# Optimization experiments

Measured on AMD Instinct MI355X. Metric: run time of the kernel, lower is better.

## Reference

```python
import jax, jax.numpy as jnp
import numpy as np
import math

TAU = 2.0
EPS = 1e-5
ALPHA = 2.0  # spikingjelly surrogate.ATan default alpha

@jax.custom_vjp
def atan_spike(x):
    return (x >= 0.0).astype(x.dtype)

def _spike_fwd(x):
    return atan_spike(x), x

def _spike_bwd(x, g):
    s = math.pi / 2.0 * ALPHA
    return (g * (ALPHA / 2.0) / (1.0 + (s * x) ** 2),)

atan_spike.defvjp(_spike_fwd, _spike_bwd)

def lif_seq(x_seq):
    # MultiStepLIFNode: v' = v + (x - v)/tau ; spike = H(v'-1) ; hard reset to v_reset=0
    def step(v, x):
        v = v + (x - v) / TAU
        s = atan_spike(v - 1.0)
        v = v * (1.0 - jax.lax.stop_gradient(s))  # detach_reset=True
        return v, s
    _, s_seq = jax.lax.scan(step, jnp.zeros_like(x_seq[0]), x_seq)
    return s_seq

def setup_inputs() -> dict:
    key = jax.random.key(0)
    kx, kw = jax.random.split(key)
    T, B, N, P, D = 4, 64, 1024, 63, 128
    x = jax.random.normal(kx, (T, B, N, P), dtype=jnp.float32)
    W = jax.random.normal(kw, (D, P), dtype=jnp.float32) * np.float32(1.0 / np.sqrt(P))
    gamma = jnp.ones((D,), dtype=jnp.float32)
    beta = jnp.zeros((D,), dtype=jnp.float32)
    return {"x": x, "W": W, "gamma": gamma, "beta": beta, "pe": 0}

def reference(x, W, gamma, beta, pe):
    # bias-free Linear: [T,B,N,P] x [D,P] -> [T,B,N,D]
    h = jnp.einsum('tbnp,dp->tbnd', x, W)
    # BatchNorm1d over channel D; training-mode batch stats over (T*B, N)
    mean = jnp.mean(h, axis=(0, 1, 2), keepdims=True)
    var = jnp.var(h, axis=(0, 1, 2), keepdims=True)  # biased, as torch BN normalization
    h = (h - mean) * jax.lax.rsqrt(var + EPS) * gamma + beta
    # multi-step LIF across T (self.pe=False -> tAPE branch skipped)
    out = lif_seq(h)  # [T,B,N,D] == original output after final transpose
    return out
```

## Files before the change

kernel.cpp:

```cpp
#include <hip/hip_runtime.h>
#include <math.h>

#define T_STEPS 4
#define R_ROWS  65536
#define M_ROWS  262144
#define P_DIM   63
#define D_DIM   128
#define PP      64

#define TILES_TOTAL (M_ROWS / 64)
#define G_CHUNKS 8

__global__ __launch_bounds__(256) void gram_kernel(const float* __restrict__ x,
                                                   double* __restrict__ partials,
                                                   int tiles_per_block) {
    __shared__ __align__(16) float xt[2][64 * PP];
    const int tid = threadIdx.x;
    const int tj = tid & 15;
    const int ti = tid >> 4;

    double dacc[4][4];
#pragma unroll
    for (int a = 0; a < 4; a++)
#pragma unroll
        for (int b = 0; b < 4; b++) dacc[a][b] = 0.0;

    if (tid < 64) {
        xt[0][tid * PP + 63] = 1.0f;
        xt[1][tid * PP + 63] = 1.0f;
    }

    const int tile0 = blockIdx.x * tiles_per_block;
    float4 reg[4];

    {
        const float4* src = (const float4*)(x + (size_t)tile0 * (64 * 63));
#pragma unroll
        for (int it = 0; it < 4; it++) {
            int k = tid + it * 256;
            reg[it] = (k < 1008) ? src[k] : make_float4(0.f, 0.f, 0.f, 0.f);
        }
    }
#pragma unroll
    for (int it = 0; it < 4; it++) {
        int k = tid + it * 256;
        if (k < 1008) {
            const float* ve = (const float*)&reg[it];
            int flat = k * 4;
#pragma unroll
            for (int e = 0; e < 4; e++) {
                int f = flat + e;
                int r = f / 63;
                int c = f - r * 63;
                xt[0][r * PP + c] = ve[e];
            }
        }
    }
    __syncthreads();

    for (int t = 0; t < tiles_per_block; t++) {
        const int cur = t & 1;
        if (t + 1 < tiles_per_block) {
            const float4* src = (const float4*)(x + (size_t)(tile0 + t + 1) * (64 * 63));
#pragma unroll
            for (int it = 0; it < 4; it++) {
                int k = tid + it * 256;
                reg[it] = (k < 1008) ? src[k] : make_float4(0.f, 0.f, 0.f, 0.f);
            }
        }

        float facc[4][4];
#pragma unroll
        for (int a = 0; a < 4; a++)
#pragma unroll
            for (int b = 0; b < 4; b++) facc[a][b] = 0.0f;

        const float* buf = xt[cur];
        for (int r = 0; r < 64; r++) {
            float4 xi = *(const float4*)&buf[r * PP + ti * 4];
            float4 xj = *(const float4*)&buf[r * PP + tj * 4];
            const float* xia = (const float*)&xi;
            const float* xja = (const float*)&xj;
#pragma unroll
            for (int a = 0; a < 4; a++)
#pragma unroll
                for (int b = 0; b < 4; b++)
                    facc[a][b] = fmaf(xia[a], xja[b], facc[a][b]);
        }
#pragma unroll
        for (int a = 0; a < 4; a++)
#pragma unroll
            for (int b = 0; b < 4; b++) dacc[a][b] += (double)facc[a][b];

        __syncthreads();
        if (t + 1 < tiles_per_block) {
            float* nbuf = xt[1 - cur];
#pragma unroll
            for (int it = 0; it < 4; it++) {
                int k = tid + it * 256;
                if (k < 1008) {
                    const float* ve = (const float*)&reg[it];
                    int flat = k * 4;
#pragma unroll
                    for (int e = 0; e < 4; e++) {
                        int f = flat + e;
                        int r = f / 63;
                        int c = f - r * 63;
                        nbuf[r * PP + c] = ve[e];
                    }
                }
            }
            __syncthreads();
        }
    }

    double* Pb = partials + (size_t)blockIdx.x * 4096;
#pragma unroll
    for (int a = 0; a < 4; a++)
#pragma unroll
        for (int b = 0; b < 4; b++)
            Pb[(ti * 4 + a) * 64 + (tj * 4 + b)] = dacc[a][b];
}

__global__ __launch_bounds__(256) void reduce_kernel(const double* __restrict__ partials,
                                                     double* __restrict__ G8,
                                                     int copies_per_chunk) {
    const int chunk = blockIdx.x >> 4;
    const int idx   = (blockIdx.x & 15) * 256 + threadIdx.x;
    const double* src = partials + (size_t)chunk * copies_per_chunk * 4096;
    double s = 0.0;
    for (int c = 0; c < copies_per_chunk; c++)
        s += src[(size_t)c * 4096 + idx];
    G8[(size_t)chunk * 4096 + idx] = s;
}

__global__ __launch_bounds__(64) void stats_kernel(const double* __restrict__ G,
                                                   const float* __restrict__ W,
                                                   const float* __restrict__ gamma,
                                                   const float* __restrict__ beta,
                                                   float* __restrict__ stats) {
    const int d = blockIdx.x;
    const int p = threadIdx.x;
    __shared__ float sW[64];
    sW[p] = (p < P_DIM) ? W[d * P_DIM + p] : 0.0f;
    __syncthreads();

    double inner = 0.0;
#pragma unroll
    for (int c = 0; c < G_CHUNKS; c++) {
        const double* Gr = G + (size_t)c * (64 * 64) + p * 64;
        for (int q = 0; q < 64; q++) inner += Gr[q] * (double)sW[q];
    }

    double contrib = (double)sW[p] * inner;
    double ex2M = contrib;
#pragma unroll
    for (int off = 32; off > 0; off >>= 1) ex2M += __shfl_down(ex2M, off, 64);
    double meanM = __shfl(inner, 63, 64);

    if (p == 0) {
        double mean = meanM / (double)M_ROWS;
        double ex2  = ex2M  / (double)M_ROWS;
        double var  = ex2 - mean * mean;
        float varf  = (float)var;
        float vpe   = varf + 1e-5f;
        float invstd = (float)(1.0 / sqrt((double)vpe));
        stats[d * 4 + 0] = (float)mean;
        stats[d * 4 + 1] = invstd;
        stats[d * 4 + 2] = gamma[d];
        stats[d * 4 + 3] = beta[d];
    }
}

#define LIF_ROWS 16
#define SW_STRIDE 132
__global__ __launch_bounds__(256) void lif_kernel(const float* __restrict__ x,
                                                  const float* __restrict__ W,
                                                  const float* __restrict__ stats,
                                                  float* __restrict__ out) {
    __shared__ __align__(16) float sw[P_DIM * SW_STRIDE];
    __shared__ __align__(16) float sx[T_STEPS * LIF_ROWS * P_DIM + 4];
    const int tid = threadIdx.x;

    for (int k = tid; k < P_DIM * D_DIM; k += 256) {
        int d = k / 63;
        int p = k - d * 63;
        sw[p * SW_STRIDE + d] = W[k];
    }

    const int r0 = blockIdx.x * LIF_ROWS;
    const int seg = tid >> 6;
    const int lane = tid & 63;
    const float4* src = (const float4*)(x + ((size_t)seg * R_ROWS + r0) * P_DIM);
    float4* dst = (float4*)sx + seg * 252;
    for (int k = lane; k < 252; k += 64) {
        dst[k] = src[k];
    }
    __syncthreads();

    const int td = tid & 31;
    const int tr = tid >> 5;
    const int d0 = td * 4;
    const int rowa = tr * 2;

    float acc[T_STEPS][2][4];
#pragma unroll
    for (int t = 0; t < T_STEPS; t++)
#pragma unroll
        for (int i = 0; i < 2; i++)
#pragma unroll
            for (int j = 0; j < 4; j++) acc[t][i][j] = 0.0f;

    for (int p = 0; p < P_DIM; p++) {
        float4 w4 = *(const float4*)&sw[p * SW_STRIDE + d0];
#pragma unroll
        for (int t = 0; t < T_STEPS; t++)
#pragma unroll
            for (int i = 0; i < 2; i++) {
                float xv = sx[(t * LIF_ROWS + rowa + i) * P_DIM + p];
                acc[t][i][0] = fmaf(xv, w4.x, acc[t][i][0]);
                acc[t][i][1] = fmaf(xv, w4.y, acc[t][i][1]);
                acc[t][i][2] = fmaf(xv, w4.z, acc[t][i][2]);
                acc[t][i][3] = fmaf(xv, w4.w, acc[t][i][3]);
            }
    }

#pragma unroll
    for (int i = 0; i < 2; i++) {
        const int row = r0 + rowa + i;
        float sval[T_STEPS][4];
#pragma unroll
        for (int j = 0; j < 4; j++) {
            float4 st = ((const float4*)stats)[d0 + j];
            float v = 0.0f;
#pragma unroll
            for (int t = 0; t < T_STEPS; t++) {
                float hn = (acc[t][i][j] - st.x) * st.y;
                hn = hn * st.z;
                hn = hn + st.w;
                v = v + (hn - v) * 0.5f;
                float s = (v >= 1.0f) ? 1.0f : 0.0f;
                sval[t][j] = s;
                if (s != 0.0f) v = 0.0f;
            }
        }
#pragma unroll
        for (int t = 0; t < T_STEPS; t++) {
            float4 o = make_float4(sval[t][0], sval[t][1], sval[t][2], sval[t][3]);
            *(float4*)&out[((size_t)t * R_ROWS + row) * D_DIM + d0] = o;
        }
    }
}

extern "C" void kernel_launch(void* const* d_in, const int* in_sizes, int n_in,
                              void* d_out, int out_size, void* d_ws, size_t ws_size,
                              hipStream_t stream) {
    const float* x     = (const float*)d_in[0];
    const float* W     = (const float*)d_in[1];
    const float* gamma = (const float*)d_in[2];
    const float* beta  = (const float*)d_in[3];
    float* out = (float*)d_out;

    const size_t fixed = (size_t)G_CHUNKS * 4096 * 8 + 4096;
    int nparts = 512;
    while (nparts > 64 && (size_t)nparts * 4096 * 8 + fixed > ws_size) nparts >>= 1;
    const int tiles_per_block = TILES_TOTAL / nparts;

    double* partials = (double*)d_ws;
    double* G8       = (double*)((char*)d_ws + (size_t)nparts * 4096 * 8);
    float*  stats    = (float*)((char*)G8 + (size_t)G_CHUNKS * 4096 * 8);

    gram_kernel<<<nparts, 256, 0, stream>>>(x, partials, tiles_per_block);
    reduce_kernel<<<G_CHUNKS * 16, 256, 0, stream>>>(partials, G8, nparts / G_CHUNKS);
    stats_kernel<<<D_DIM, 64, 0, stream>>>(G8, W, gamma, beta, stats);
    lif_kernel<<<R_ROWS / LIF_ROWS, 256, 0, stream>>>(x, W, stats, out);
}
```

Measured before the change: 290.7 us.

## Enlarge LIF tile to 32 rows with swizzled float4 LDS loads of x

The LIF GEMM kernel now handles 32 rows per block, and each thread computes 8 output columns instead of 4. x is stored in LDS padded to 64 columns with an XOR swizzle, so the inner loop can read float4 vectors of x and four p-values of W per step. This cuts LDS read instructions per FMA and halves the grid size. It also doubles the accumulator registers (64 floats) and the per-block LDS footprint, which may lower occupancy. W is transposed through LDS using an extra staging pass.

```diff
diff --git a/kernel.cpp b/kernel.cpp
--- a/kernel.cpp
+++ b/kernel.cpp
@@ -172,65 +172,116 @@
     }
 }
 
-#define LIF_ROWS 16
-#define SW_STRIDE 132
-__global__ __launch_bounds__(256) void lif_kernel(const float* __restrict__ x,
-                                                  const float* __restrict__ W,
-                                                  const float* __restrict__ stats,
-                                                  float* __restrict__ out) {
-    __shared__ __align__(16) float sw[P_DIM * SW_STRIDE];
-    __shared__ __align__(16) float sx[T_STEPS * LIF_ROWS * P_DIM + 4];
+#define LIF_ROWS 32
+__global__ __launch_bounds__(256, 2) void lif_kernel(const float* __restrict__ x,
+                                                     const float* __restrict__ W,
+                                                     const float* __restrict__ stats,
+                                                     float* __restrict__ out) {
+    __shared__ __align__(16) float sw[P_DIM * D_DIM];
+    __shared__ __align__(16) float sx[T_STEPS * LIF_ROWS * 64];
     const int tid = threadIdx.x;
 
+    for (int k = tid; k < P_DIM * D_DIM; k += 256) sx[k] = W[k];
+    __syncthreads();
     for (int k = tid; k < P_DIM * D_DIM; k += 256) {
-        int d = k / 63;
-        int p = k - d * 63;
-        sw[p * SW_STRIDE + d] = W[k];
-    }
+        int p = k >> 7;
+        int d = k & 127;
+        sw[k] = sx[d * P_DIM + p];
+    }
+    __syncthreads();
 
     const int r0 = blockIdx.x * LIF_ROWS;
     const int seg = tid >> 6;
     const int lane = tid & 63;
     const float4* src = (const float4*)(x + ((size_t)seg * R_ROWS + r0) * P_DIM);
-    float4* dst = (float4*)sx + seg * 252;
-    for (int k = lane; k < 252; k += 64) {
-        dst[k] = src[k];
-    }
-    __syncthreads();
-
-    const int td = tid & 31;
-    const int tr = tid >> 5;
-    const int d0 = td * 4;
-    const int rowa = tr * 2;
-
-    float acc[T_STEPS][2][4];
+    for (int k = lane; k < 504; k += 64) {
+        float4 v = src[k];
+        const float* ve = (const float*)&v;
+        int flat = k * 4;
+#pragma unroll
+        for (int e = 0; e < 4; e++) {
+            int f = flat + e;
+            int r = f / 63;
+            int c = f - r * 63;
+            int cs = (((c >> 2) ^ ((r >> 1) & 3)) << 2) | (c & 3);
+            sx[(seg * LIF_ROWS + r) * 64 + cs] = ve[e];
+        }
+    }
+    __syncthreads();
+
+    const int td = tid & 15;
+    const int tr = tid >> 4;
+    const int d0 = td * 8;
+    const int lr0 = tr * 2;
+    const int sq0 = (lr0 >> 1) & 3;
+
+    float acc[T_STEPS][2][8];
 #pragma unroll
     for (int t = 0; t < T_STEPS; t++)
 #pragma unroll
         for (int i = 0; i < 2; i++)
 #pragma unroll
-            for (int j = 0; j < 4; j++) acc[t][i][j] = 0.0f;
-
-    for (int p = 0; p < P_DIM; p++) {
-        float4 w4 = *(const float4*)&sw[p * SW_STRIDE + d0];
+            for (int j = 0; j < 8; j++) acc[t][i][j] = 0.0f;
+
+    for (int pq = 0; pq < 15; pq++) {
+        const int p0 = pq * 4;
+        float4 w[4][2];
+#pragma unroll
+        for (int pp = 0; pp < 4; pp++)
+#pragma unroll
+            for (int h = 0; h < 2; h++)
+                w[pp][h] = *(const float4*)&sw[(p0 + pp) * D_DIM + d0 + h * 4];
+
+        const int xq = (pq ^ sq0) << 2;
 #pragma unroll
         for (int t = 0; t < T_STEPS; t++)
 #pragma unroll
             for (int i = 0; i < 2; i++) {
-                float xv = sx[(t * LIF_ROWS + rowa + i) * P_DIM + p];
-                acc[t][i][0] = fmaf(xv, w4.x, acc[t][i][0]);
-                acc[t][i][1] = fmaf(xv, w4.y, acc[t][i][1]);
-                acc[t][i][2] = fmaf(xv, w4.z, acc[t][i][2]);
-                acc[t][i][3] = fmaf(xv, w4.w, acc[t][i][3]);
+                float4 xv = *(const float4*)&sx[(t * LIF_ROWS + lr0 + i) * 64 + xq];
+                const float xe[4] = {xv.x, xv.y, xv.z, xv.w};
+                float* a = acc[t][i];
+#pragma unroll
+                for (int pp = 0; pp < 4; pp++) {
+#pragma unroll
+                    for (int h = 0; h < 2; h++) {
+                        const float4 ww = w[pp][h];
+                        a[h * 4 + 0] = fmaf(xe[pp], ww.x, a[h * 4 + 0]);
+                        a[h * 4 + 1] = fmaf(xe[pp], ww.y, a[h * 4 + 1]);
+                        a[h * 4 + 2] = fmaf(xe[pp], ww.z, a[h * 4 + 2]);
+                        a[h * 4 + 3] = fmaf(xe[pp], ww.w, a[h * 4 + 3]);
+                    }
+                }
+            }
+    }
+
+#pragma unroll
+    for (int p = 60; p < 63; p++) {
+        float4 wA = *(const float4*)&sw[p * D_DIM + d0];
+        float4 wB = *(const float4*)&sw[p * D_DIM + d0 + 4];
+        const int cs = ((15 ^ sq0) << 2) | (p & 3);
+#pragma unroll
+        for (int t = 0; t < T_STEPS; t++)
+#pragma unroll
+            for (int i = 0; i < 2; i++) {
+                float xv = sx[(t * LIF_ROWS + lr0 + i) * 64 + cs];
+                float* a = acc[t][i];
+                a[0] = fmaf(xv, wA.x, a[0]);
+                a[1] = fmaf(xv, wA.y, a[1]);
+                a[2] = fmaf(xv, wA.z, a[2]);
+                a[3] = fmaf(xv, wA.w, a[3]);
+                a[4] = fmaf(xv, wB.x, a[4]);
+                a[5] = fmaf(xv, wB.y, a[5]);
+                a[6] = fmaf(xv, wB.z, a[6]);
+                a[7] = fmaf(xv, wB.w, a[7]);
             }
     }
 
 #pragma unroll
     for (int i = 0; i < 2; i++) {
-        const int row = r0 + rowa + i;
-        float sval[T_STEPS][4];
-#pragma unroll
-        for (int j = 0; j < 4; j++) {
+        const int row = r0 + lr0 + i;
+        float sval[T_STEPS][8];
+#pragma unroll
+        for (int j = 0; j < 8; j++) {
             float4 st = ((const float4*)stats)[d0 + j];
             float v = 0.0f;
 #pragma unroll
@@ -246,8 +297,9 @@
         }
 #pragma unroll
         for (int t = 0; t < T_STEPS; t++) {
-            float4 o = make_float4(sval[t][0], sval[t][1], sval[t][2], sval[t][3]);
-            *(float4*)&out[((size_t)t * R_ROWS + row) * D_DIM + d0] = o;
+            float* ob = &out[((size_t)t * R_ROWS + row) * D_DIM + d0];
+            *(float4*)ob       = make_float4(sval[t][0], sval[t][1], sval[t][2], sval[t][3]);
+            *(float4*)(ob + 4) = make_float4(sval[t][4], sval[t][5], sval[t][6], sval[t][7]);
         }
     }
 }
```

Measured after the change: 291.7 us. No clear change (+0.3%).

## Use packed FP32 FMA with row-interleaved shared layout and nontemporal memory ops

Applied to the files above, without the earlier changes.

Shared-memory x is re-laid out so the two rows a thread handles are interleaved per column. Each thread can then feed v_pk_fma_f32 through inline asm with op_sel broadcast of the weights, halving FMA instruction count and cutting LDS reads via wider vector loads. Global loads of x and stores of spikes become nontemporal to reduce cache pollution. The scatter during staging makes the load loop costlier, and the inline asm limits compiler scheduling.

```diff
diff --git a/kernel.cpp b/kernel.cpp
--- a/kernel.cpp
+++ b/kernel.cpp
@@ -10,6 +10,18 @@
 
 #define TILES_TOTAL (M_ROWS / 64)
 #define G_CHUNKS 8
+
+typedef float v2f __attribute__((ext_vector_type(2)));
+typedef float v4f __attribute__((ext_vector_type(4)));
+
+__device__ __forceinline__ void pk_fma_wlo(v2f& acc, v2f x, v2f w) {
+    asm("v_pk_fma_f32 %0, %1, %2, %0 op_sel:[0,0,0] op_sel_hi:[1,0,1]"
+        : "+v"(acc) : "v"(x), "v"(w));
+}
+__device__ __forceinline__ void pk_fma_whi(v2f& acc, v2f x, v2f w) {
+    asm("v_pk_fma_f32 %0, %1, %2, %0 op_sel:[0,1,0] op_sel_hi:[1,1,1]"
+        : "+v"(acc) : "v"(x), "v"(w));
+}
 
 __global__ __launch_bounds__(256) void gram_kernel(const float* __restrict__ x,
                                                    double* __restrict__ partials,
@@ -179,7 +191,7 @@
                                                   const float* __restrict__ stats,
                                                   float* __restrict__ out) {
     __shared__ __align__(16) float sw[P_DIM * SW_STRIDE];
-    __shared__ __align__(16) float sx[T_STEPS * LIF_ROWS * P_DIM + 4];
+    __shared__ __align__(16) float sx[T_STEPS * 8 * 128];
     const int tid = threadIdx.x;
 
     for (int k = tid; k < P_DIM * D_DIM; k += 256) {
@@ -191,40 +203,72 @@
     const int r0 = blockIdx.x * LIF_ROWS;
     const int seg = tid >> 6;
     const int lane = tid & 63;
-    const float4* src = (const float4*)(x + ((size_t)seg * R_ROWS + r0) * P_DIM);
-    float4* dst = (float4*)sx + seg * 252;
+    const v4f* src = (const v4f*)(x + ((size_t)seg * R_ROWS + r0) * P_DIM);
     for (int k = lane; k < 252; k += 64) {
-        dst[k] = src[k];
+        v4f v = __builtin_nontemporal_load(&src[k]);
+        int flat = k * 4;
+#pragma unroll
+        for (int e = 0; e < 4; e++) {
+            int f = flat + e;
+            int r = f / 63;
+            int c = f - r * 63;
+            sx[((seg * 8 + (r >> 1)) * 64 + c) * 2 + (r & 1)] = v[e];
+        }
     }
     __syncthreads();
 
     const int td = tid & 31;
     const int tr = tid >> 5;
     const int d0 = td * 4;
+
+    v2f acc2[T_STEPS][4];
+#pragma unroll
+    for (int t = 0; t < T_STEPS; t++)
+#pragma unroll
+        for (int j = 0; j < 4; j++) acc2[t][j] = (v2f){0.0f, 0.0f};
+
+    for (int pq = 0; pq < 15; pq++) {
+        const int p0 = pq * 4;
+        v2f w01[4], w23[4];
+#pragma unroll
+        for (int pp = 0; pp < 4; pp++) {
+            w01[pp] = *(const v2f*)&sw[(p0 + pp) * SW_STRIDE + d0];
+            w23[pp] = *(const v2f*)&sw[(p0 + pp) * SW_STRIDE + d0 + 2];
+        }
+#pragma unroll
+        for (int t = 0; t < T_STEPS; t++) {
+            const int base = ((t * 8 + tr) * 64 + p0) * 2;
+            v4f xa = *(const v4f*)&sx[base];
+            v4f xb = *(const v4f*)&sx[base + 4];
+            v2f xp[4];
+            xp[0] = (v2f){xa.x, xa.y};
+            xp[1] = (v2f){xa.z, xa.w};
+            xp[2] = (v2f){xb.x, xb.y};
+            xp[3] = (v2f){xb.z, xb.w};
+#pragma unroll
+            for (int pp = 0; pp < 4; pp++) {
+                pk_fma_wlo(acc2[t][0], xp[pp], w01[pp]);
+                pk_fma_whi(acc2[t][1], xp[pp], w01[pp]);
+                pk_fma_wlo(acc2[t][2], xp[pp], w23[pp]);
+                pk_fma_whi(acc2[t][3], xp[pp], w23[pp]);
+            }
+        }
+    }
+#pragma unroll
+    for (int p = 60; p < 63; p++) {
+        v2f w01 = *(const v2f*)&sw[p * SW_STRIDE + d0];
+        v2f w23 = *(const v2f*)&sw[p * SW_STRIDE + d0 + 2];
+#pragma unroll
+        for (int t = 0; t < T_STEPS; t++) {
+            v2f xp = *(const v2f*)&sx[((t * 8 + tr) * 64 + p) * 2];
+            pk_fma_wlo(acc2[t][0], xp, w01);
+            pk_fma_whi(acc2[t][1], xp, w01);
+            pk_fma_wlo(acc2[t][2], xp, w23);
+            pk_fma_whi(acc2[t][3], xp, w23);
+        }
+    }
+
     const int rowa = tr * 2;
-
-    float acc[T_STEPS][2][4];
-#pragma unroll
-    for (int t = 0; t < T_STEPS; t++)
-#pragma unroll
-        for (int i = 0; i < 2; i++)
-#pragma unroll
-            for (int j = 0; j < 4; j++) acc[t][i][j] = 0.0f;
-
-    for (int p = 0; p < P_DIM; p++) {
-        float4 w4 = *(const float4*)&sw[p * SW_STRIDE + d0];
-#pragma unroll
-        for (int t = 0; t < T_STEPS; t++)
-#pragma unroll
-            for (int i = 0; i < 2; i++) {
-                float xv = sx[(t * LIF_ROWS + rowa + i) * P_DIM + p];
-                acc[t][i][0] = fmaf(xv, w4.x, acc[t][i][0]);
-                acc[t][i][1] = fmaf(xv, w4.y, acc[t][i][1]);
-                acc[t][i][2] = fmaf(xv, w4.z, acc[t][i][2]);
-                acc[t][i][3] = fmaf(xv, w4.w, acc[t][i][3]);
-            }
-    }
-
 #pragma unroll
     for (int i = 0; i < 2; i++) {
         const int row = r0 + rowa + i;
@@ -235,7 +279,7 @@
             float v = 0.0f;
 #pragma unroll
             for (int t = 0; t < T_STEPS; t++) {
-                float hn = (acc[t][i][j] - st.x) * st.y;
+                float hn = (acc2[t][j][i] - st.x) * st.y;
                 hn = hn * st.z;
                 hn = hn + st.w;
                 v = v + (hn - v) * 0.5f;
@@ -246,8 +290,9 @@
         }
 #pragma unroll
         for (int t = 0; t < T_STEPS; t++) {
-            float4 o = make_float4(sval[t][0], sval[t][1], sval[t][2], sval[t][3]);
-            *(float4*)&out[((size_t)t * R_ROWS + row) * D_DIM + d0] = o;
+            v4f o = {sval[t][0], sval[t][1], sval[t][2], sval[t][3]};
+            __builtin_nontemporal_store(
+                o, (v4f*)&out[((size_t)t * R_ROWS + row) * D_DIM + d0]);
         }
     }
 }
```

Measured after the change: 288.1 us. About the same (-0.9%).
